# Kernel tuning notes

Measured on AMD Instinct MI355X. Metric: run time of the kernel, lower is better.

The kernel has to match this reference:

```python
import jax, jax.numpy as jnp
import numpy as np

DIM = 1024
NUM_HEADS = 16
HEAD_DIM = DIM // NUM_HEADS
TAU = 1.0
LAMBDA_JUMP = 0.6
LAMBDA_LOCAL = 0.4
MIN_ENTROPY = 0.5
WINDOW = 3
EPS = 1e-10


def local_diffusion_kernel(seq_len, strength, window=WINDOW):
    # Banded Gaussian kernel, row-normalized. [S, S]
    i = jnp.arange(seq_len)
    d = i[:, None] - i[None, :]
    k = jnp.where(jnp.abs(d) <= window,
                  jnp.exp(-(d.astype(jnp.float32) ** 2) / (2.0 * strength ** 2)),
                  0.0)
    return k / (k.sum(axis=-1, keepdims=True) + EPS)


def setup_inputs() -> dict:
    key = jax.random.key(0)
    ks = jax.random.split(key, 9)
    scale = 0.02
    x = jax.random.normal(ks[0], (2, 2048, DIM), dtype=jnp.float32)
    Wq = jax.random.normal(ks[1], (DIM, DIM), dtype=jnp.float32) * scale
    bq = jax.random.normal(ks[2], (DIM,), dtype=jnp.float32) * scale
    Wk = jax.random.normal(ks[3], (DIM, DIM), dtype=jnp.float32) * scale
    bk = jax.random.normal(ks[4], (DIM,), dtype=jnp.float32) * scale
    Wv = jax.random.normal(ks[5], (DIM, DIM), dtype=jnp.float32) * scale
    bv = jax.random.normal(ks[6], (DIM,), dtype=jnp.float32) * scale
    Wo = jax.random.normal(ks[7], (DIM, DIM), dtype=jnp.float32) * scale
    bo = jax.random.normal(ks[8], (DIM,), dtype=jnp.float32) * scale
    return {"x": x, "Wq": Wq, "bq": bq, "Wk": Wk, "bk": bk,
            "Wv": Wv, "bv": bv, "Wo": Wo, "bo": bo}


def reference(x, Wq, bq, Wk, bk, Wv, bv, Wo, bo):
    B, S, D = x.shape
    H, hd = NUM_HEADS, HEAD_DIM
    # torch Linear: y = x @ W.T + b
    Q = (x @ Wq.T + bq).reshape(B, S, H, hd).transpose(0, 2, 1, 3)  # [B,H,S,hd]
    K = (x @ Wk.T + bk).reshape(B, S, H, hd).transpose(0, 2, 1, 3)
    V = (x @ Wv.T + bv).reshape(B, S, H, hd).transpose(0, 2, 1, 3)

    scores = jnp.einsum('bhqd,bhkd->bhqk', Q, K) / (TAU * np.sqrt(hd).astype(np.float32))
    A = jax.nn.softmax(scores, axis=-1)  # [B,H,S,S]

    # Per-row entropy gating (detach-based in torch: forward value is unchanged)
    entropy = -jnp.sum(A * jnp.log(A + EPS), axis=-1, keepdims=True)
    stable = jax.lax.stop_gradient((entropy >= MIN_ENTROPY).astype(A.dtype))
    A = stable * A + (1.0 - stable) * jax.lax.stop_gradient(A)

    L = local_diffusion_kernel(S, LAMBDA_LOCAL)  # [S,S]
    A_stable = LAMBDA_JUMP * A + (1.0 - LAMBDA_JUMP) * L[None, None, :, :]

    out = jnp.einsum('bhqk,bhkd->bhqd', A_stable, V)  # [B,H,S,hd]
    out = out.transpose(0, 2, 1, 3).reshape(B, S, D)
    return out @ Wo.T + bo
```

## Files before the change

kernel.cpp:

```cpp
#include <hip/hip_runtime.h>
#include <math.h>

typedef __bf16 bf16x8 __attribute__((ext_vector_type(8)));
typedef float f32x4 __attribute__((ext_vector_type(4)));

namespace {
constexpr int DIMC = 1024, NH = 16, HD = 64, SEQ = 2048;
constexpr float SCL2 = 0.1803368801f;
}

__device__ __forceinline__ unsigned short f2b(float f) {
  unsigned u = __float_as_uint(f);
  return (unsigned short)((u + 0x7fffu + ((u >> 16) & 1u)) >> 16);
}
__device__ __forceinline__ float b2f(unsigned short s) {
  return __uint_as_float((unsigned)s << 16);
}
__device__ __forceinline__ unsigned cvtpk(float lo, float hi) {
  unsigned r;
  asm("v_cvt_pk_bf16_f32 %0, %1, %2" : "=v"(r) : "v"(lo), "v"(hi));
  return r;
}
__device__ __forceinline__ void gld16(void* l, const void* g) {
  __builtin_amdgcn_global_load_lds(
      (const __attribute__((address_space(1))) void*)g,
      (__attribute__((address_space(3))) void*)l, 16, 0, 0);
}

__global__ __launch_bounds__(256)
void cvt_bf16(const float* __restrict__ in, unsigned short* __restrict__ out, int n8) {
  int i = blockIdx.x * 256 + threadIdx.x;
  if (i >= n8) return;
  const float4* in4 = (const float4*)in;
  float4 a = in4[2 * i], b = in4[2 * i + 1];
  union { unsigned short u[8]; uint4 v; } r;
  r.u[0] = f2b(a.x); r.u[1] = f2b(a.y); r.u[2] = f2b(a.z); r.u[3] = f2b(a.w);
  r.u[4] = f2b(b.x); r.u[5] = f2b(b.y); r.u[6] = f2b(b.z); r.u[7] = f2b(b.w);
  ((uint4*)out)[i] = r.v;
}

__global__ __launch_bounds__(256)
void cvt_w4(const float* __restrict__ w0, const float* __restrict__ w1,
            const float* __restrict__ w2, const float* __restrict__ w3,
            unsigned short* __restrict__ out) {
  const int which = blockIdx.y;
  const float* src = which == 0 ? w0 : which == 1 ? w1 : which == 2 ? w2 : w3;
  unsigned short* dst = out + (size_t)which * 1048576;
  int i = blockIdx.x * 256 + threadIdx.x;
  const float4* in4 = (const float4*)src;
  float4 a = in4[2 * i], b = in4[2 * i + 1];
  union { unsigned short u[8]; uint4 v; } r;
  r.u[0] = f2b(a.x); r.u[1] = f2b(a.y); r.u[2] = f2b(a.z); r.u[3] = f2b(a.w);
  r.u[4] = f2b(b.x); r.u[5] = f2b(b.y); r.u[6] = f2b(b.z); r.u[7] = f2b(b.w);
  ((uint4*)dst)[i] = r.v;
}

template<int MODE>
__device__ __forceinline__
void gemm_tile128(const unsigned short* __restrict__ A, const unsigned short* __restrict__ W,
                  const float* __restrict__ bias, void* __restrict__ Cout,
                  int bm, int bn, float scl, char* As, char* Bs) {
  const int tid = threadIdx.x, lane = tid & 63, w = tid >> 6;
  const int p = lane & 15, g = lane >> 4;
  const int wr = w >> 1, wc = w & 1;
  const int sr = tid >> 2, sc = (tid & 3) * 8;

  f32x4 acc[4][4];
#pragma unroll
  for (int mf = 0; mf < 4; ++mf)
#pragma unroll
    for (int nf = 0; nf < 4; ++nf)
      acc[mf][nf] = (f32x4){0.f, 0.f, 0.f, 0.f};

  const size_t arow0 = (size_t)(bm + sr) * DIMC + sc;
  const size_t arow1 = (size_t)(bm + 64 + sr) * DIMC + sc;
  const size_t brow0 = (size_t)(bn + sr) * DIMC + sc;
  const size_t brow1 = (size_t)(bn + 64 + sr) * DIMC + sc;

  for (int k0 = 0; k0 < DIMC; k0 += 32) {
    __syncthreads();
    gld16(&As[tid * 16],        &A[arow0 + k0]);
    gld16(&As[4096 + tid * 16], &A[arow1 + k0]);
    gld16(&Bs[tid * 16],        &W[brow0 + k0]);
    gld16(&Bs[4096 + tid * 16], &W[brow1 + k0]);
    __syncthreads();
    bf16x8 af[4], bfr[4];
#pragma unroll
    for (int mf = 0; mf < 4; ++mf)
      af[mf] = *(const bf16x8*)&As[(wr * 64 + mf * 16 + p) * 64 + g * 16];
#pragma unroll
    for (int nf = 0; nf < 4; ++nf)
      bfr[nf] = *(const bf16x8*)&Bs[(wc * 64 + nf * 16 + p) * 64 + g * 16];
#pragma unroll
    for (int mf = 0; mf < 4; ++mf)
#pragma unroll
      for (int nf = 0; nf < 4; ++nf)
        acc[mf][nf] = __builtin_amdgcn_mfma_f32_16x16x32_bf16(af[mf], bfr[nf], acc[mf][nf], 0, 0, 0);
  }

#pragma unroll
  for (int nf = 0; nf < 4; ++nf) {
    const int cg = bn + wc * 64 + nf * 16 + p;
    const float bv = bias[cg & (DIMC - 1)];
#pragma unroll
    for (int mf = 0; mf < 4; ++mf) {
#pragma unroll
      for (int j = 0; j < 4; ++j) {
        const int rg = bm + wr * 64 + mf * 16 + g * 4 + j;
        const float v = (acc[mf][nf][j] + bv) * scl;
        if (MODE == 0) {
          ((float*)Cout)[(size_t)rg * DIMC + cg] = v;
        } else {
          const int bb = rg >> 11, ss = rg & (SEQ - 1);
          const int hh = cg >> 6, dd = cg & (HD - 1);
          ((unsigned short*)Cout)[(((size_t)(bb * NH + hh) * SEQ + ss) * HD) + dd] = f2b(v);
        }
      }
    }
  }
}

__global__ __launch_bounds__(256, 2)
void gemm_qkv(const unsigned short* __restrict__ A, const unsigned short* __restrict__ Wall,
              const float* __restrict__ bq, const float* __restrict__ bk,
              const float* __restrict__ bv, unsigned short* __restrict__ Out) {
  __shared__ char As[8192];
  __shared__ char Bs[8192];
  const int which = blockIdx.z;
  const unsigned short* W = Wall + (size_t)which * 1048576;
  const float* bias = which == 0 ? bq : which == 1 ? bk : bv;
  unsigned short* Cout = Out + (size_t)which * 4194304;
  const float scl = which == 0 ? SCL2 : 1.0f;
  gemm_tile128<1>(A, W, bias, Cout, blockIdx.x * 128, blockIdx.y * 128, scl, As, Bs);
}

__global__ __launch_bounds__(256, 2)
void gemm_out(const unsigned short* __restrict__ A, const unsigned short* __restrict__ W,
              const float* __restrict__ bias, float* __restrict__ Cout) {
  __shared__ char As[8192];
  __shared__ char Bs[4096];
  const int tid = threadIdx.x, lane = tid & 63, w = tid >> 6;
  const int p = lane & 15, g = lane >> 4;
  const int wr = w >> 1, wc = w & 1;
  const int bm = blockIdx.x * 128, bn = blockIdx.y * 64;
  const int sr = tid >> 2, sc = (tid & 3) * 8;

  f32x4 acc[4][2];
#pragma unroll
  for (int mf = 0; mf < 4; ++mf)
#pragma unroll
    for (int nf = 0; nf < 2; ++nf)
      acc[mf][nf] = (f32x4){0.f, 0.f, 0.f, 0.f};

  const size_t arow0 = (size_t)(bm + sr) * DIMC + sc;
  const size_t arow1 = (size_t)(bm + 64 + sr) * DIMC + sc;
  const size_t brow  = (size_t)(bn + sr) * DIMC + sc;

  for (int k0 = 0; k0 < DIMC; k0 += 32) {
    __syncthreads();
    gld16(&As[tid * 16],        &A[arow0 + k0]);
    gld16(&As[4096 + tid * 16], &A[arow1 + k0]);
    gld16(&Bs[tid * 16],        &W[brow + k0]);
    __syncthreads();
    bf16x8 af[4], bfr[2];
#pragma unroll
    for (int mf = 0; mf < 4; ++mf)
      af[mf] = *(const bf16x8*)&As[(wr * 64 + mf * 16 + p) * 64 + g * 16];
#pragma unroll
    for (int nf = 0; nf < 2; ++nf)
      bfr[nf] = *(const bf16x8*)&Bs[(wc * 32 + nf * 16 + p) * 64 + g * 16];
#pragma unroll
    for (int mf = 0; mf < 4; ++mf)
#pragma unroll
      for (int nf = 0; nf < 2; ++nf)
        acc[mf][nf] = __builtin_amdgcn_mfma_f32_16x16x32_bf16(af[mf], bfr[nf], acc[mf][nf], 0, 0, 0);
  }

#pragma unroll
  for (int nf = 0; nf < 2; ++nf) {
    const int cg = bn + wc * 32 + nf * 16 + p;
    const float bv = bias[cg];
#pragma unroll
    for (int mf = 0; mf < 4; ++mf) {
#pragma unroll
      for (int j = 0; j < 4; ++j) {
        const int rg = bm + wr * 64 + mf * 16 + g * 4 + j;
        Cout[(size_t)rg * DIMC + cg] = acc[mf][nf][j] + bv;
      }
    }
  }
}

__global__ __launch_bounds__(256, 2)
void attn_fused(const unsigned short* __restrict__ Q, const unsigned short* __restrict__ K,
                const unsigned short* __restrict__ V, unsigned short* __restrict__ Y) {
  __shared__ char lds[73728];
  const int tid = threadIdx.x, lane = tid & 63, w = tid >> 6;
  const int p = lane & 15, g = lane >> 4;
  const int bh = blockIdx.x, b = bh >> 4, h = bh & 15;
  const int q0 = blockIdx.y * 128;
  const int qg = w & 1, kst = w >> 1;
  const int qwv = q0 + qg * 64;
  const size_t base = (size_t)bh * SEQ * HD;
  const unsigned short* Qp = Q + base;
  const unsigned short* Kp = K + base;
  const unsigned short* Vp = V + base;

  char* myPl = lds + w * 16384;
  char* myVt = lds + w * 16384 + 8192;

  union Vu { bf16x8 v; unsigned short u[8]; };

  bf16x8 qf[4][2];
#pragma unroll
  for (int mi = 0; mi < 4; ++mi)
#pragma unroll
    for (int ks = 0; ks < 2; ++ks)
      qf[mi][ks] = *(const bf16x8*)&Qp[(size_t)(qwv + mi * 16 + p) * HD + ks * 32 + g * 8];

  bf16x8 ones8;
  {
    union { unsigned short u[8]; bf16x8 v; } o;
#pragma unroll
    for (int e = 0; e < 8; ++e) o.u[e] = (p == 0) ? (unsigned short)0x3F80 : (unsigned short)0;
    ones8 = o.v;
  }

  const int kp = lane & 31, dgrp = lane >> 5;
  const unsigned short* kA = Kp + (size_t)kst * 1024 * HD + (size_t)p * HD + g * 8;
  const unsigned short* vP = Vp + (size_t)kst * 1024 * HD + (size_t)(2 * kp) * HD + dgrp * 8;

  const int swz = (p & 7) << 4;
  int pwCol[4], sCol[2], colE[8];
#pragma unroll
  for (int nf = 0; nf < 4; ++nf) pwCol[nf] = (nf * 32 + g * 8) ^ swz;
#pragma unroll
  for (int ks = 0; ks < 2; ++ks) sCol[ks] = (ks * 64 + g * 16) ^ swz;
#pragma unroll
  for (int e = 0; e < 8; ++e) colE[e] = (kp * 4) ^ (e << 4);
  char* vtD = myVt + dgrp * 1024;

  f32x4 o2[4][4];
  f32x4 ol[4];
#pragma unroll
  for (int mi = 0; mi < 4; ++mi) {
#pragma unroll
    for (int nf = 0; nf < 4; ++nf)
      o2[mi][nf] = (f32x4){0.f, 0.f, 0.f, 0.f};
    ol[mi] = (f32x4){0.f, 0.f, 0.f, 0.f};
  }

  bf16x8 kf[4][2];
  Vu vv[4][2];

  auto loadKV = [&]() {
    kf[0][0] = *(const bf16x8*)(kA + 0);    kf[0][1] = *(const bf16x8*)(kA + 32);
    kf[1][0] = *(const bf16x8*)(kA + 1024); kf[1][1] = *(const bf16x8*)(kA + 1056);
    kf[2][0] = *(const bf16x8*)(kA + 2048); kf[2][1] = *(const bf16x8*)(kA + 2080);
    kf[3][0] = *(const bf16x8*)(kA + 3072); kf[3][1] = *(const bf16x8*)(kA + 3104);
#pragma unroll
    for (int c = 0; c < 4; ++c) {
      vv[c][0].v = *(const bf16x8*)(vP + c * 16);
      vv[c][1].v = *(const bf16x8*)(vP + HD + c * 16);
    }
    kA += 4096; vP += 4096;
  };
  auto scoreStage = [&]() {
#pragma unroll
    for (int mi = 0; mi < 4; ++mi) {
      f32x4 s[4];
#pragma unroll
      for (int nf = 0; nf < 4; ++nf) s[nf] = (f32x4){0.f, 0.f, 0.f, 0.f};
      __builtin_amdgcn_s_setprio(1);
#pragma unroll
      for (int nf = 0; nf < 4; ++nf)
#pragma unroll
        for (int ks = 0; ks < 2; ++ks)
          s[nf] = __builtin_amdgcn_mfma_f32_16x16x32_bf16(kf[nf][ks], qf[mi][ks], s[nf], 0, 0, 0);
      __builtin_amdgcn_s_setprio(0);
#pragma unroll
      for (int nf = 0; nf < 4; ++nf)
#pragma unroll
        for (int j = 0; j < 4; ++j)
          s[nf][j] = exp2f(s[nf][j]);
#pragma unroll
      for (int nf = 0; nf < 4; ++nf) {
        uint2 val;
        val.x = cvtpk(s[nf][0], s[nf][1]);
        val.y = cvtpk(s[nf][2], s[nf][3]);
        *(uint2*)(myPl + p * 128 + mi * 2048 + pwCol[nf]) = val;
      }
    }
  };
  auto stageVt = [&]() {
#pragma unroll
    for (int c = 0; c < 4; ++c)
#pragma unroll
      for (int e = 0; e < 8; ++e) {
        const unsigned val = (unsigned)vv[c][0].u[e] | ((unsigned)vv[c][1].u[e] << 16);
        *(unsigned*)(vtD + c * 2048 + e * 128 + colE[e]) = val;
      }
  };
  auto pv = [&]() {
    bf16x8 vb[4][2];
#pragma unroll
    for (int nfd = 0; nfd < 4; ++nfd)
#pragma unroll
      for (int ks = 0; ks < 2; ++ks)
        vb[nfd][ks] = *(const bf16x8*)(myVt + p * 128 + nfd * 2048 + sCol[ks]);
#pragma unroll
    for (int mi = 0; mi < 4; ++mi) {
      bf16x8 pf[2];
#pragma unroll
      for (int ks = 0; ks < 2; ++ks)
        pf[ks] = *(const bf16x8*)(myPl + p * 128 + mi * 2048 + sCol[ks]);
      __builtin_amdgcn_s_setprio(1);
#pragma unroll
      for (int nfd = 0; nfd < 4; ++nfd)
#pragma unroll
        for (int ks = 0; ks < 2; ++ks)
          o2[mi][nfd] = __builtin_amdgcn_mfma_f32_16x16x32_bf16(vb[nfd][ks], pf[ks], o2[mi][nfd], 0, 0, 0);
#pragma unroll
      for (int ks = 0; ks < 2; ++ks)
        ol[mi] = __builtin_amdgcn_mfma_f32_16x16x32_bf16(ones8, pf[ks], ol[mi], 0, 0, 0);
      __builtin_amdgcn_s_setprio(0);
    }
  };

  loadKV();
  scoreStage();
  stageVt();
  for (int kt = 1; kt < 16; ++kt) {
    loadKV();
    pv();
    scoreStage();
    stageVt();
  }
  pv();

  if (kst == 1) {
    char* dst = lds + w * 16384;
#pragma unroll
    for (int mi = 0; mi < 4; ++mi)
#pragma unroll
      for (int nfd = 0; nfd < 4; ++nfd)
        *(f32x4*)(dst + (mi * 4 + nfd) * 1024 + lane * 16) = o2[mi][nfd];
    char* dsl = lds + 65536 + (w - 2) * 4096;
#pragma unroll
    for (int mi = 0; mi < 4; ++mi)
      *(f32x4*)(dsl + mi * 1024 + lane * 16) = ol[mi];
  }
  __syncthreads();
  if (kst == 1) return;

  {
    const char* src = lds + (w + 2) * 16384;
#pragma unroll
    for (int mi = 0; mi < 4; ++mi)
#pragma unroll
      for (int nfd = 0; nfd < 4; ++nfd)
        o2[mi][nfd] += *(const f32x4*)(src + (mi * 4 + nfd) * 1024 + lane * 16);
    const char* sl = lds + 65536 + w * 4096;
#pragma unroll
    for (int mi = 0; mi < 4; ++mi)
      ol[mi] += *(const f32x4*)(sl + mi * 1024 + lane * 16);
  }

  const float e1 = 4.3936934e-2f, e2 = 3.7266532e-6f, e3 = 6.1019804e-13f;
  const float lwv[4] = {1.f, e1, e2, e3};
#pragma unroll
  for (int mi = 0; mi < 4; ++mi) {
    const int q = qwv + mi * 16 + p;
    const float lq = __shfl(ol[mi][0], p);
    const float inv = 0.6f / lq;
    float wsum = 0.f;
#pragma unroll
    for (int dd = -3; dd <= 3; ++dd) {
      const int kk = q + dd;
      if (kk >= 0 && kk < SEQ) wsum += lwv[dd < 0 ? -dd : dd];
    }
    const float wn = 0.4f / (wsum + 1e-10f);
#pragma unroll
    for (int nfd = 0; nfd < 4; ++nfd) {
      const int d0 = nfd * 16 + g * 4;
      float loc[4] = {0.f, 0.f, 0.f, 0.f};
#pragma unroll
      for (int dd = -3; dd <= 3; ++dd) {
        const int kk = q + dd;
        if (kk >= 0 && kk < SEQ) {
          const uint2 lv = *(const uint2*)&Vp[(size_t)kk * HD + d0];
          const float wt = lwv[dd < 0 ? -dd : dd];
          loc[0] = fmaf(wt, b2f((unsigned short)lv.x), loc[0]);
          loc[1] = fmaf(wt, b2f((unsigned short)(lv.x >> 16)), loc[1]);
          loc[2] = fmaf(wt, b2f((unsigned short)lv.y), loc[2]);
          loc[3] = fmaf(wt, b2f((unsigned short)(lv.y >> 16)), loc[3]);
        }
      }
      uint2 st;
      st.x = cvtpk(o2[mi][nfd][0] * inv + loc[0] * wn, o2[mi][nfd][1] * inv + loc[1] * wn);
      st.y = cvtpk(o2[mi][nfd][2] * inv + loc[2] * wn, o2[mi][nfd][3] * inv + loc[3] * wn);
      *(uint2*)&Y[((size_t)(b * SEQ + q)) * DIMC + h * HD + d0] = st;
    }
  }
}

extern "C" void kernel_launch(void* const* d_in, const int* in_sizes, int n_in,
                              void* d_out, int out_size, void* d_ws, size_t ws_size,
                              hipStream_t stream) {
  (void)in_sizes; (void)n_in; (void)out_size; (void)ws_size;
  const float* x  = (const float*)d_in[0];
  const float* Wq = (const float*)d_in[1];
  const float* bq = (const float*)d_in[2];
  const float* Wk = (const float*)d_in[3];
  const float* bk = (const float*)d_in[4];
  const float* Wv = (const float*)d_in[5];
  const float* bv = (const float*)d_in[6];
  const float* Wo = (const float*)d_in[7];
  const float* bo = (const float*)d_in[8];

  char* ws = (char*)d_ws;
  unsigned short* xb  = (unsigned short*)(ws);
  unsigned short* Wqb = (unsigned short*)(ws + 8388608);
  unsigned short* Wob = (unsigned short*)(ws + 14680064);
  unsigned short* Qh  = (unsigned short*)(ws + 16777216);
  unsigned short* Kh  = (unsigned short*)(ws + 25165824);
  unsigned short* Vh  = (unsigned short*)(ws + 33554432);
  unsigned short* Yb  = (unsigned short*)(ws + 41943040);

  dim3 blk(256);
  cvt_bf16<<<2048, blk, 0, stream>>>(x, xb, 524288);
  cvt_w4<<<dim3(512, 4), blk, 0, stream>>>(Wq, Wk, Wv, Wo, Wqb);

  gemm_qkv<<<dim3(32, 8, 3), blk, 0, stream>>>(xb, Wqb, bq, bk, bv, Qh);

  attn_fused<<<dim3(32, 16), blk, 0, stream>>>(Qh, Kh, Vh, Yb);

  gemm_out<<<dim3(32, 16), blk, 0, stream>>>(Yb, Wob, bo, (float*)d_out);
}
```

Measured before the change: 148.2 us.

## Restructure attention into 8-warp blocks with shared, double-buffered K/V LDS staging

```diff
diff --git a/kernel.cpp b/kernel.cpp
--- a/kernel.cpp
+++ b/kernel.cpp
@@ -59,7 +59,7 @@
 __device__ __forceinline__
 void gemm_tile128(const unsigned short* __restrict__ A, const unsigned short* __restrict__ W,
                   const float* __restrict__ bias, void* __restrict__ Cout,
-                  int bm, int bn, float scl, char* As, char* Bs) {
+                  int bm, int bn, float scl, bool kswz, char* As, char* Bs) {
   const int tid = threadIdx.x, lane = tid & 63, w = tid >> 6;
   const int p = lane & 15, g = lane >> 4;
   const int wr = w >> 1, wc = w & 1;
@@ -112,7 +112,9 @@
           ((float*)Cout)[(size_t)rg * DIMC + cg] = v;
         } else {
           const int bb = rg >> 11, ss = rg & (SEQ - 1);
-          const int hh = cg >> 6, dd = cg & (HD - 1);
+          const int hh = cg >> 6;
+          int dd = cg & (HD - 1);
+          if (kswz) dd ^= (ss & 7) << 3;
           ((unsigned short*)Cout)[(((size_t)(bb * NH + hh) * SEQ + ss) * HD) + dd] = f2b(v);
         }
       }
@@ -131,7 +133,7 @@
   const float* bias = which == 0 ? bq : which == 1 ? bk : bv;
   unsigned short* Cout = Out + (size_t)which * 4194304;
   const float scl = which == 0 ? SCL2 : 1.0f;
-  gemm_tile128<1>(A, W, bias, Cout, blockIdx.x * 128, blockIdx.y * 128, scl, As, Bs);
+  gemm_tile128<1>(A, W, bias, Cout, blockIdx.x * 128, blockIdx.y * 128, scl, which == 1, As, Bs);
 }
 
 __global__ __launch_bounds__(256, 2)
@@ -191,32 +193,28 @@
   }
 }
 
-__global__ __launch_bounds__(256, 2)
+__global__ __launch_bounds__(512, 4)
 void attn_fused(const unsigned short* __restrict__ Q, const unsigned short* __restrict__ K,
                 const unsigned short* __restrict__ V, unsigned short* __restrict__ Y) {
-  __shared__ char lds[73728];
+  __shared__ char Kl[2][8192];
+  __shared__ char Vt[2][8192];
+  __shared__ char Pl[16384];
   const int tid = threadIdx.x, lane = tid & 63, w = tid >> 6;
   const int p = lane & 15, g = lane >> 4;
   const int bh = blockIdx.x, b = bh >> 4, h = bh & 15;
   const int q0 = blockIdx.y * 128;
-  const int qg = w & 1, kst = w >> 1;
-  const int qwv = q0 + qg * 64;
+  const int qwv = q0 + w * 16;
   const size_t base = (size_t)bh * SEQ * HD;
   const unsigned short* Qp = Q + base;
   const unsigned short* Kp = K + base;
   const unsigned short* Vp = V + base;
 
-  char* myPl = lds + w * 16384;
-  char* myVt = lds + w * 16384 + 8192;
-
   union Vu { bf16x8 v; unsigned short u[8]; };
 
-  bf16x8 qf[4][2];
-#pragma unroll
-  for (int mi = 0; mi < 4; ++mi)
-#pragma unroll
-    for (int ks = 0; ks < 2; ++ks)
-      qf[mi][ks] = *(const bf16x8*)&Qp[(size_t)(qwv + mi * 16 + p) * HD + ks * 32 + g * 8];
+  bf16x8 qf[2];
+#pragma unroll
+  for (int ks = 0; ks < 2; ++ks)
+    qf[ks] = *(const bf16x8*)&Qp[(size_t)(qwv + p) * HD + ks * 32 + g * 8];
 
   bf16x8 ones8;
   {
@@ -226,152 +224,131 @@
     ones8 = o.v;
   }
 
-  const int kp = lane & 31, dgrp = lane >> 5;
-  const unsigned short* kA = Kp + (size_t)kst * 1024 * HD + (size_t)p * HD + g * 8;
-  const unsigned short* vP = Vp + (size_t)kst * 1024 * HD + (size_t)(2 * kp) * HD + dgrp * 8;
+  const unsigned short* kSrc = Kp + (size_t)(tid >> 3) * HD + (tid & 7) * 8;
+  const int kp = tid & 31, vd0 = ((tid >> 5) & 7) * 8;
+  const bool vload = tid < 256;
+  const unsigned short* vSrc = Vp + (size_t)(2 * kp) * HD + vd0;
 
   const int swz = (p & 7) << 4;
-  int pwCol[4], sCol[2], colE[8];
+  int sCol[2], pwCol[4], colE[8];
+#pragma unroll
+  for (int ks = 0; ks < 2; ++ks) sCol[ks] = (ks * 64 + g * 16) ^ swz;
 #pragma unroll
   for (int nf = 0; nf < 4; ++nf) pwCol[nf] = (nf * 32 + g * 8) ^ swz;
 #pragma unroll
-  for (int ks = 0; ks < 2; ++ks) sCol[ks] = (ks * 64 + g * 16) ^ swz;
-#pragma unroll
   for (int e = 0; e < 8; ++e) colE[e] = (kp * 4) ^ (e << 4);
-  char* vtD = myVt + dgrp * 1024;
-
-  f32x4 o2[4][4];
-  f32x4 ol[4];
-#pragma unroll
-  for (int mi = 0; mi < 4; ++mi) {
+
+  f32x4 o2[4];
+  f32x4 ol;
+#pragma unroll
+  for (int nf = 0; nf < 4; ++nf) o2[nf] = (f32x4){0.f, 0.f, 0.f, 0.f};
+  ol = (f32x4){0.f, 0.f, 0.f, 0.f};
+
+  Vu v0A, v1A, v0B, v1B;
+
+  auto gldK = [&](int par, int kb) {
+    gld16(&Kl[par][tid * 16], kSrc + (size_t)kb * HD);
+  };
+  auto loadV = [&](Vu& a0, Vu& a1, int kb) {
+    if (vload) {
+      a0.v = *(const bf16x8*)(vSrc + (size_t)kb * HD);
+      a1.v = *(const bf16x8*)(vSrc + (size_t)(kb + 1) * HD);
+    }
+  };
+  auto writeV = [&](int par, Vu& a0, Vu& a1) {
+    if (vload) {
+      char* vtp = &Vt[par][0] + vd0 * 128;
+#pragma unroll
+      for (int e = 0; e < 8; ++e) {
+        const unsigned val = (unsigned)a0.u[e] | ((unsigned)a1.u[e] << 16);
+        *(unsigned*)(vtp + e * 128 + colE[e]) = val;
+      }
+    }
+  };
+  auto qkt_sm_stage = [&](int par) {
+    const char* klp = &Kl[par][0] + p * 128;
+    bf16x8 kf[4][2];
 #pragma unroll
     for (int nf = 0; nf < 4; ++nf)
-      o2[mi][nf] = (f32x4){0.f, 0.f, 0.f, 0.f};
-    ol[mi] = (f32x4){0.f, 0.f, 0.f, 0.f};
-  }
-
-  bf16x8 kf[4][2];
-  Vu vv[4][2];
-
-  auto loadKV = [&]() {
-    kf[0][0] = *(const bf16x8*)(kA + 0);    kf[0][1] = *(const bf16x8*)(kA + 32);
-    kf[1][0] = *(const bf16x8*)(kA + 1024); kf[1][1] = *(const bf16x8*)(kA + 1056);
-    kf[2][0] = *(const bf16x8*)(kA + 2048); kf[2][1] = *(const bf16x8*)(kA + 2080);
-    kf[3][0] = *(const bf16x8*)(kA + 3072); kf[3][1] = *(const bf16x8*)(kA + 3104);
-#pragma unroll
-    for (int c = 0; c < 4; ++c) {
-      vv[c][0].v = *(const bf16x8*)(vP + c * 16);
-      vv[c][1].v = *(const bf16x8*)(vP + HD + c * 16);
-    }
-    kA += 4096; vP += 4096;
+#pragma unroll
+      for (int ks = 0; ks < 2; ++ks)
+        kf[nf][ks] = *(const bf16x8*)(klp + nf * 2048 + sCol[ks]);
+    f32x4 s[4];
+#pragma unroll
+    for (int nf = 0; nf < 4; ++nf) s[nf] = (f32x4){0.f, 0.f, 0.f, 0.f};
+    __builtin_amdgcn_s_setprio(1);
+#pragma unroll
+    for (int nf = 0; nf < 4; ++nf)
+#pragma unroll
+      for (int ks = 0; ks < 2; ++ks)
+        s[nf] = __builtin_amdgcn_mfma_f32_16x16x32_bf16(kf[nf][ks], qf[ks], s[nf], 0, 0, 0);
+    __builtin_amdgcn_s_setprio(0);
+#pragma unroll
+    for (int nf = 0; nf < 4; ++nf)
+#pragma unroll
+      for (int j = 0; j < 4; ++j)
+        s[nf][j] = exp2f(s[nf][j]);
+    char* plp = &Pl[0] + w * 2048 + p * 128;
+#pragma unroll
+    for (int nf = 0; nf < 4; ++nf) {
+      uint2 val;
+      val.x = cvtpk(s[nf][0], s[nf][1]);
+      val.y = cvtpk(s[nf][2], s[nf][3]);
+      *(uint2*)(plp + pwCol[nf]) = val;
+    }
   };
-  auto scoreStage = [&]() {
-#pragma unroll
-    for (int mi = 0; mi < 4; ++mi) {
-      f32x4 s[4];
-#pragma unroll
-      for (int nf = 0; nf < 4; ++nf) s[nf] = (f32x4){0.f, 0.f, 0.f, 0.f};
-      __builtin_amdgcn_s_setprio(1);
-#pragma unroll
-      for (int nf = 0; nf < 4; ++nf)
-#pragma unroll
-        for (int ks = 0; ks < 2; ++ks)
-          s[nf] = __builtin_amdgcn_mfma_f32_16x16x32_bf16(kf[nf][ks], qf[mi][ks], s[nf], 0, 0, 0);
-      __builtin_amdgcn_s_setprio(0);
-#pragma unroll
-      for (int nf = 0; nf < 4; ++nf)
-#pragma unroll
-        for (int j = 0; j < 4; ++j)
-          s[nf][j] = exp2f(s[nf][j]);
-#pragma unroll
-      for (int nf = 0; nf < 4; ++nf) {
-        uint2 val;
-        val.x = cvtpk(s[nf][0], s[nf][1]);
-        val.y = cvtpk(s[nf][2], s[nf][3]);
-        *(uint2*)(myPl + p * 128 + mi * 2048 + pwCol[nf]) = val;
-      }
-    }
+  auto pv = [&](int par) {
+    const char* plp = &Pl[0] + w * 2048 + p * 128;
+    bf16x8 pf[2];
+#pragma unroll
+    for (int ks = 0; ks < 2; ++ks)
+      pf[ks] = *(const bf16x8*)(plp + sCol[ks]);
+    const char* vtp = &Vt[par][0] + p * 128;
+    bf16x8 vb[4][2];
+#pragma unroll
+    for (int nfd = 0; nfd < 4; ++nfd)
+#pragma unroll
+      for (int ks = 0; ks < 2; ++ks)
+        vb[nfd][ks] = *(const bf16x8*)(vtp + nfd * 2048 + sCol[ks]);
+    __builtin_amdgcn_s_setprio(1);
+#pragma unroll
+    for (int nfd = 0; nfd < 4; ++nfd)
+#pragma unroll
+      for (int ks = 0; ks < 2; ++ks)
+        o2[nfd] = __builtin_amdgcn_mfma_f32_16x16x32_bf16(vb[nfd][ks], pf[ks], o2[nfd], 0, 0, 0);
+#pragma unroll
+    for (int ks = 0; ks < 2; ++ks)
+      ol = __builtin_amdgcn_mfma_f32_16x16x32_bf16(ones8, pf[ks], ol, 0, 0, 0);
+    __builtin_amdgcn_s_setprio(0);
   };
-  auto stageVt = [&]() {
-#pragma unroll
-    for (int c = 0; c < 4; ++c)
-#pragma unroll
-      for (int e = 0; e < 8; ++e) {
-        const unsigned val = (unsigned)vv[c][0].u[e] | ((unsigned)vv[c][1].u[e] << 16);
-        *(unsigned*)(vtD + c * 2048 + e * 128 + colE[e]) = val;
-      }
-  };
-  auto pv = [&]() {
-    bf16x8 vb[4][2];
-#pragma unroll
-    for (int nfd = 0; nfd < 4; ++nfd)
-#pragma unroll
-      for (int ks = 0; ks < 2; ++ks)
-        vb[nfd][ks] = *(const bf16x8*)(myVt + p * 128 + nfd * 2048 + sCol[ks]);
-#pragma unroll
-    for (int mi = 0; mi < 4; ++mi) {
-      bf16x8 pf[2];
-#pragma unroll
-      for (int ks = 0; ks < 2; ++ks)
-        pf[ks] = *(const bf16x8*)(myPl + p * 128 + mi * 2048 + sCol[ks]);
-      __builtin_amdgcn_s_setprio(1);
-#pragma unroll
-      for (int nfd = 0; nfd < 4; ++nfd)
-#pragma unroll
-        for (int ks = 0; ks < 2; ++ks)
-          o2[mi][nfd] = __builtin_amdgcn_mfma_f32_16x16x32_bf16(vb[nfd][ks], pf[ks], o2[mi][nfd], 0, 0, 0);
-#pragma unroll
-      for (int ks = 0; ks < 2; ++ks)
-        ol[mi] = __builtin_amdgcn_mfma_f32_16x16x32_bf16(ones8, pf[ks], ol[mi], 0, 0, 0);
-      __builtin_amdgcn_s_setprio(0);
-    }
-  };
-
-  loadKV();
-  scoreStage();
-  stageVt();
-  for (int kt = 1; kt < 16; ++kt) {
-    loadKV();
-    pv();
-    scoreStage();
-    stageVt();
-  }
-  pv();
-
-  if (kst == 1) {
-    char* dst = lds + w * 16384;
-#pragma unroll
-    for (int mi = 0; mi < 4; ++mi)
-#pragma unroll
-      for (int nfd = 0; nfd < 4; ++nfd)
-        *(f32x4*)(dst + (mi * 4 + nfd) * 1024 + lane * 16) = o2[mi][nfd];
-    char* dsl = lds + 65536 + (w - 2) * 4096;
-#pragma unroll
-    for (int mi = 0; mi < 4; ++mi)
-      *(f32x4*)(dsl + mi * 1024 + lane * 16) = ol[mi];
-  }
+
+  gldK(0, 0);
+  loadV(v0A, v1A, 0);
   __syncthreads();
-  if (kst == 1) return;
-
-  {
-    const char* src = lds + (w + 2) * 16384;
-#pragma unroll
-    for (int mi = 0; mi < 4; ++mi)
-#pragma unroll
-      for (int nfd = 0; nfd < 4; ++nfd)
-        o2[mi][nfd] += *(const f32x4*)(src + (mi * 4 + nfd) * 1024 + lane * 16);
-    const char* sl = lds + 65536 + w * 4096;
-#pragma unroll
-    for (int mi = 0; mi < 4; ++mi)
-      ol[mi] += *(const f32x4*)(sl + mi * 1024 + lane * 16);
+
+  for (int it = 0; it < 16; ++it) {
+    const int t0 = 2 * it;
+    gldK(1, (t0 + 1) * 64);
+    loadV(v0B, v1B, (t0 + 1) * 64);
+    qkt_sm_stage(0);
+    writeV(0, v0A, v1A);
+    __syncthreads();
+    pv(0);
+    if (it < 15) {
+      gldK(0, (t0 + 2) * 64);
+      loadV(v0A, v1A, (t0 + 2) * 64);
+    }
+    qkt_sm_stage(1);
+    writeV(1, v0B, v1B);
+    __syncthreads();
+    pv(1);
   }
 
   const float e1 = 4.3936934e-2f, e2 = 3.7266532e-6f, e3 = 6.1019804e-13f;
   const float lwv[4] = {1.f, e1, e2, e3};
-#pragma unroll
-  for (int mi = 0; mi < 4; ++mi) {
-    const int q = qwv + mi * 16 + p;
-    const float lq = __shfl(ol[mi][0], p);
+  {
+    const int q = qwv + p;
+    const float lq = __shfl(ol[0], p);
     const float inv = 0.6f / lq;
     float wsum = 0.f;
 #pragma unroll
@@ -397,8 +374,8 @@
         }
       }
       uint2 st;
-      st.x = cvtpk(o2[mi][nfd][0] * inv + loc[0] * wn, o2[mi][nfd][1] * inv + loc[1] * wn);
-      st.y = cvtpk(o2[mi][nfd][2] * inv + loc[2] * wn, o2[mi][nfd][3] * inv + loc[3] * wn);
+      st.x = cvtpk(o2[nfd][0] * inv + loc[0] * wn, o2[nfd][1] * inv + loc[1] * wn);
+      st.y = cvtpk(o2[nfd][2] * inv + loc[2] * wn, o2[nfd][3] * inv + loc[3] * wn);
       *(uint2*)&Y[((size_t)(b * SEQ + q)) * DIMC + h * HD + d0] = st;
     }
   }
@@ -433,7 +410,7 @@
 
   gemm_qkv<<<dim3(32, 8, 3), blk, 0, stream>>>(xb, Wqb, bq, bk, bv, Qh);
 
-  attn_fused<<<dim3(32, 16), blk, 0, stream>>>(Qh, Kh, Vh, Yb);
+  attn_fused<<<dim3(32, 16), dim3(512), 0, stream>>>(Qh, Kh, Vh, Yb);
 
   gemm_out<<<dim3(32, 16), blk, 0, stream>>>(Yb, Wob, bo, (float*)d_out);
 }
```

Result: faster. 129.4 us (-12.7%).
